# Kernel optimization log

Measured on AMD Instinct MI355X. Metric: run time of the kernel, lower is better.

The kernel has to match this reference:

```python
import jax, jax.numpy as jnp
import numpy as np
from jax import lax

B, T, V = 128, 100, 100000
ED, MD, H = 300, 50, 512   # embed_dim, mask_dim, l_hidden_size
HH = H // 2                # per-direction GRU hidden
C1 = 0.1
C2 = 0.1


def _reverse_valid(x, lens):
    # reverse the valid prefix of each sequence (emulates packed-sequence reverse dir)
    t = jnp.arange(x.shape[1])[None, :]
    idx = jnp.where(t < lens[:, None], lens[:, None] - 1 - t, t)
    return jnp.take_along_axis(x, idx[:, :, None], axis=1)


def _gru_dir(x, valid, lens, wih, whh, bih, bhh, reverse):
    # x: [B,T,Din], valid: [B,T] bool. PyTorch GRU cell math, packed-seq semantics:
    # state frozen and output zeroed at padded steps.
    if reverse:
        x = _reverse_valid(x, lens)
    h0 = jnp.zeros((x.shape[0], whh.shape[1]), x.dtype)
    def step(h, inp):
        xt, mt = inp
        gi = xt @ wih.T + bih
        gh = h @ whh.T + bhh
        ir, iz, inn = jnp.split(gi, 3, axis=-1)
        hr, hz, hn = jnp.split(gh, 3, axis=-1)
        r = jax.nn.sigmoid(ir + hr)
        z = jax.nn.sigmoid(iz + hz)
        n = jnp.tanh(inn + r * hn)
        hnew = (1.0 - z) * n + z * h
        hnew = jnp.where(mt[:, None], hnew, h)
        return hnew, jnp.where(mt[:, None], hnew, 0.0)
    _, out = lax.scan(step, h0, (x.transpose(1, 0, 2), valid.T))
    out = out.transpose(1, 0, 2)
    if reverse:
        out = _reverse_valid(out, lens)
    return out


def _crf_marginals(feats, L, trans):
    # linear-chain CRF forward-backward marginals, 2 latent states; feats [T,2], valid length L
    Tm = feats.shape[0]
    def fstep(alpha, inp):
        ft, t = inp
        new = jax.nn.logsumexp(alpha[:, None] + trans, axis=0) + ft
        a = jnp.where(t < L, new, alpha)
        return a, a
    a0 = feats[0]
    _, rest = lax.scan(fstep, a0, (feats[1:], jnp.arange(1, Tm)))
    alphas = jnp.concatenate([a0[None], rest], axis=0)
    logZ = jax.nn.logsumexp(alphas[L - 1])
    def bstep(beta, inp):
        fn, t = inp
        cand = jax.nn.logsumexp(trans + (fn + beta)[None, :], axis=1)
        b = jnp.where(t >= L - 1, jnp.zeros_like(cand), cand)
        return b, b
    _, brev = lax.scan(bstep, jnp.zeros((2,), feats.dtype), (feats[1:][::-1], jnp.arange(Tm - 2, -1, -1)))
    betas = jnp.concatenate([brev[::-1], jnp.zeros((1, 2), feats.dtype)], axis=0)
    marg = jnp.exp(alphas + betas - logZ)
    return jnp.where(jnp.arange(Tm)[:, None] < L, marg, 0.0)


def setup_inputs():
    key = jax.random.key(0)
    ks = jax.random.split(key, 30)
    s = 0.08
    inp = {}
    inp["sents"] = jax.random.randint(ks[0], (B, T), 0, V, dtype=jnp.int32)
    lens = jnp.sort(jax.random.randint(ks[1], (B,), 5, T + 1, dtype=jnp.int32))[::-1]
    inp["lens"] = lens
    t = jnp.arange(T)[None, :]
    start = (lens // 3)[:, None]
    inp["masks"] = ((t >= start) & (t < start + 3)).astype(jnp.int32)
    inp["labels"] = jax.random.randint(ks[2], (B,), 0, 3, dtype=jnp.int32)
    inp["word_emb"] = jax.random.normal(ks[3], (V, ED)) * s
    inp["mask_emb"] = jax.random.normal(ks[4], (2, MD)) * s
    i = 5
    for l, din in ((0, ED + MD), (1, H)):
        for d in ("f", "b"):
            inp[f"gru{l}{d}_wih"] = jax.random.normal(ks[i], (3 * HH, din)) * s; i += 1
            inp[f"gru{l}{d}_whh"] = jax.random.normal(ks[i], (3 * HH, HH)) * s; i += 1
            inp[f"gru{l}{d}_bih"] = jnp.zeros((3 * HH,))
            inp[f"gru{l}{d}_bhh"] = jnp.zeros((3 * HH,))
    inp["conv_w"] = jax.random.normal(ks[i], (H, H, 3)) * s; i += 1
    inp["conv_b"] = jnp.zeros((H,))
    inp["tri_w"] = jax.random.normal(ks[i], (2, 2 * H)) * s; i += 1
    inp["tri_b"] = jnp.zeros((2,))
    inp["trans"] = jax.random.normal(ks[i], (2, 2)) * s; i += 1
    inp["lab_w"] = jax.random.normal(ks[i], (3, H)) * s; i += 1
    inp["lab_b"] = jnp.zeros((3,))
    return inp


def _forward(sents, masks, labels, lens, word_emb, mask_emb, gru_params, conv_w, conv_b, tri_w, tri_b, trans, lab_w, lab_b):
    x = jnp.concatenate([word_emb[sents], mask_emb[masks]], axis=-1)  # SimpleCat
    valid = jnp.arange(T)[None, :] < lens[:, None]
    for layer in range(2):  # 2-layer bidirectional GRU
        pf, pb = gru_params[2 * layer], gru_params[2 * layer + 1]
        f = _gru_dir(x, valid, lens, *pf, False)
        b = _gru_dir(x, valid, lens, *pb, True)
        x = jnp.concatenate([f, b], axis=-1)
    context = jax.nn.relu(
        lax.conv_general_dilated(x, conv_w.transpose(2, 1, 0), (1,), [(1, 1)],
                                 dimension_numbers=("NWC", "WIO", "NWC")) + conv_b)
    mf = masks.astype(context.dtype)
    avg = jnp.einsum("bt,bth->bh", mf, context) / mf.sum(1, keepdims=True)  # target avg emb
    ctx1 = jnp.concatenate([context, jnp.broadcast_to(avg[:, None, :], context.shape)], axis=-1)
    tri = ctx1 @ tri_w.T + tri_b  # [B,T,2]
    marg = jax.vmap(_crf_marginals, in_axes=(0, 0, None))(tri, lens, trans)
    sp = marg[:, :, 1]  # select polarity, zeroed beyond each sent_len
    sent_v = jnp.einsum("bt,bth->bh", sp, context)
    gamma = jnp.clip(sp.sum(1) / 2.0, 1e-4, 1e5)
    scores = (sent_v / gamma[:, None]) @ lab_w.T + lab_b
    logp = jax.nn.log_softmax(scores, axis=-1)
    cls_loss = -jnp.mean(jnp.take_along_axis(logp, labels[:, None], axis=1))  # NLLLoss
    s_norm = jnp.mean(sp.sum(1))  # mean L1 norm of nonneg marginals
    pena = jax.nn.relu(trans[1, 0] - trans[0, 0]) + jax.nn.relu(trans[0, 1] - trans[1, 1])
    return jnp.stack([cls_loss, C1 * pena + C2 * s_norm])


def reference(sents, masks, labels, lens, word_emb, mask_emb, gru0f_wih, gru0f_whh, gru0f_bih, gru0f_bhh, gru0b_wih, gru0b_whh, gru0b_bih, gru0b_bhh, gru1f_wih, gru1f_whh, gru1f_bih, gru1f_bhh, gru1b_wih, gru1b_whh, gru1b_bih, gru1b_bhh, conv_w, conv_b, tri_w, tri_b, trans, lab_w, lab_b):
    gp = ((gru0f_wih, gru0f_whh, gru0f_bih, gru0f_bhh),
          (gru0b_wih, gru0b_whh, gru0b_bih, gru0b_bhh),
          (gru1f_wih, gru1f_whh, gru1f_bih, gru1f_bhh),
          (gru1b_wih, gru1b_whh, gru1b_bih, gru1b_bhh))
    return _forward(sents, masks, labels, lens, word_emb, mask_emb, gp, conv_w, conv_b, tri_w, tri_b, trans, lab_w, lab_b)
```

## Files before the change

kernel.cpp:

```cpp
#include <hip/hip_runtime.h>
#include <hip/hip_bf16.h>
#include <stdint.h>


#define TT 100
#define BB 128

typedef short s16;
typedef unsigned int u32;
typedef __attribute__((ext_vector_type(8))) short s16x8;
typedef __attribute__((ext_vector_type(4))) float f32x4;
typedef __attribute__((ext_vector_type(2))) float f32x2;

__device__ __forceinline__ float bf2f(s16 s) {
  return __uint_as_float(((unsigned)(unsigned short)s) << 16);
}
__device__ __forceinline__ s16 f2bf(float f) {
  __hip_bfloat16 h = __float2bfloat16(f);
  return *(s16*)&h;
}
__device__ __forceinline__ float sigf(float x) { return 1.f / (1.f + __expf(-x)); }
__device__ __forceinline__ float tanhfast(float x) { return 2.f / (1.f + __expf(-2.f * x)) - 1.f; }
__device__ __forceinline__ float lse2(float a, float b) {
  float m = fmaxf(a, b);
  return m + logf(expf(a - m) + expf(b - m));
}

__global__ void k_prep(const float* __restrict__ wih0f, const float* __restrict__ wih0b,
                       const float* __restrict__ wih1f, const float* __restrict__ wih1b,
                       const float* __restrict__ whh0f, const float* __restrict__ whh0b,
                       const float* __restrict__ whh1f, const float* __restrict__ whh1b,
                       const float* __restrict__ convw,
                       const int* __restrict__ sents, const int* __restrict__ masks,
                       const float* __restrict__ wemb, const float* __restrict__ memb,
                       s16* __restrict__ cwih0f, s16* __restrict__ cwih0b,
                       s16* __restrict__ cwih1f, s16* __restrict__ cwih1b,
                       s16* __restrict__ wf0f, s16* __restrict__ wf0b,
                       s16* __restrict__ wf1f, s16* __restrict__ wf1b,
                       s16* __restrict__ w2, s16* __restrict__ x0,
                       uint4* __restrict__ x2z) {
  const int stride = gridDim.x * 256;
  const int base = blockIdx.x * 256 + threadIdx.x;

  for (int idx = base; idx < 768 * 352; idx += stride) {
    int n = idx / 352, k = idx % 352;
    cwih0f[idx] = (k < 350) ? f2bf(wih0f[n * 350 + k]) : (s16)0;
    cwih0b[idx] = (k < 350) ? f2bf(wih0b[n * 350 + k]) : (s16)0;
  }
  for (int idx = base; idx < 393216; idx += stride) {
    cwih1f[idx] = f2bf(wih1f[idx]);
    cwih1b[idx] = f2bf(wih1b[idx]);
  }
  for (int idx = base; idx < 196608; idx += stride) {
    int w = idx / 24576, rem = idx % 24576;
    int f = rem / 512, rem2 = rem % 512;
    int l = rem2 / 8, i = rem2 % 8;
    int nt = f / 8, kt = f % 8;
    int src = (96 * w + 16 * nt + (l & 15)) * 256 + 32 * kt + 8 * (l >> 4) + i;
    wf0f[idx] = f2bf(whh0f[src]);
    wf0b[idx] = f2bf(whh0b[src]);
    wf1f[idx] = f2bf(whh1f[src]);
    wf1b[idx] = f2bf(whh1b[src]);
  }
  for (int idx = base; idx < 786432; idx += stride) {
    int o = idx / 1536, c = idx % 1536;
    int w = c / 512, i = c % 512;
    w2[idx] = f2bf(convw[o * 1536 + i * 3 + w]);
  }
  for (int idx = base; idx < BB * TT * 352; idx += stride) {
    int c = idx % 352, bt = idx / 352;
    float v;
    if (c < 300)      v = wemb[(size_t)sents[bt] * 300 + c];
    else if (c < 350) v = memb[masks[bt] * 50 + (c - 300)];
    else              v = 0.f;
    x0[idx] = f2bf(v);
  }
  for (int idx = base; idx < 819200; idx += stride)
    x2z[idx] = make_uint4(0u, 0u, 0u, 0u);
}

__global__ __launch_bounds__(256) void k_gemm(const s16* __restrict__ A, const s16* __restrict__ Bm,
                                              s16* __restrict__ C, int K, int ldA, int ldB, int ldC,
                                              const float* __restrict__ bias, int relu) {
  __shared__ s16 As[128 * 32];
  __shared__ s16 Bs[128 * 32];
  const int t = threadIdx.x, w = t >> 6, l = t & 63;
  const size_t m0 = (size_t)blockIdx.x * 128, n0 = (size_t)blockIdx.y * 128;
  f32x4 zero = {0.f, 0.f, 0.f, 0.f};
  f32x4 acc[4][4];
#pragma unroll
  for (int i = 0; i < 4; ++i)
#pragma unroll
    for (int j = 0; j < 4; ++j) acc[i][j] = zero;

  for (int kb = 0; kb < K; kb += 32) {
    __syncthreads();
    {
      const s16* gA = A + (m0 + (t >> 1)) * (size_t)ldA + kb + 16 * (t & 1);
      *(s16x8*)&As[(t >> 1) * 32 + 16 * (t & 1)]     = *(const s16x8*)gA;
      *(s16x8*)&As[(t >> 1) * 32 + 16 * (t & 1) + 8] = *(const s16x8*)(gA + 8);
      const s16* gB = Bm + (n0 + (t >> 1)) * (size_t)ldB + kb + 16 * (t & 1);
      *(s16x8*)&Bs[(t >> 1) * 32 + 16 * (t & 1)]     = *(const s16x8*)gB;
      *(s16x8*)&Bs[(t >> 1) * 32 + 16 * (t & 1) + 8] = *(const s16x8*)(gB + 8);
    }
    __syncthreads();
    s16x8 a[4], b[4];
#pragma unroll
    for (int i = 0; i < 4; ++i)
      a[i] = *(const s16x8*)&As[(64 * (w >> 1) + 16 * i + (l & 15)) * 32 + 8 * (l >> 4)];
#pragma unroll
    for (int j = 0; j < 4; ++j)
      b[j] = *(const s16x8*)&Bs[(64 * (w & 1) + 16 * j + (l & 15)) * 32 + 8 * (l >> 4)];
#pragma unroll
    for (int i = 0; i < 4; ++i)
#pragma unroll
      for (int j = 0; j < 4; ++j)
        acc[i][j] = __builtin_amdgcn_mfma_f32_16x16x32_bf16(a[i], b[j], acc[i][j], 0, 0, 0);
  }
#pragma unroll
  for (int i = 0; i < 4; ++i)
#pragma unroll
    for (int j = 0; j < 4; ++j)
#pragma unroll
      for (int r = 0; r < 4; ++r) {
        size_t row = m0 + 64 * (w >> 1) + 16 * i + 4 * (l >> 4) + r;
        size_t col = n0 + 64 * (w & 1) + 16 * j + (l & 15);
        float v = acc[i][j][r];
        if (bias) v += bias[col];
        if (relu) v = fmaxf(v, 0.f);
        C[row * (size_t)ldC + col] = f2bf(v);
      }
}

__global__ __launch_bounds__(512, 2) void k_gru(
    const s16* __restrict__ gi_f, const s16* __restrict__ gi_b,
    const s16* __restrict__ wf_f, const s16* __restrict__ wf_b,
    const float* __restrict__ bhh_f, const float* __restrict__ bhh_b,
    const int* __restrict__ lens, s16* __restrict__ out) {
  const int g = blockIdx.x;
  const int dir = blockIdx.y;
  const int tid = threadIdx.x, wid = tid >> 6, l = tid & 63;
  const s16* gi = dir ? gi_b : gi_f;
  const s16* wf = dir ? wf_b : wf_f;
  const float* bhh = dir ? bhh_b : bhh_f;
  const int col_off = dir ? 256 : 0;
  const int b0 = g * 4;

  __shared__ __align__(16) float gh2[16 * 772];
  __shared__ __align__(16) s16 hb[16 * 264];
  __shared__ int s_len[4];

  s16x8 wv[48];
#pragma unroll
  for (int f = 0; f < 48; ++f)
    wv[f] = *(const s16x8*)&wf[((size_t)(wid * 48 + f)) * 512 + l * 8];
  float bv[6];
#pragma unroll
  for (int nt = 0; nt < 6; ++nt) bv[nt] = bhh[96 * wid + 16 * nt + (l & 15)];

  for (int i = tid; i < 16 * 264; i += 512) hb[i] = 0;
  if (tid < 4) s_len[tid] = lens[b0 + tid];
  __syncthreads();

  const int smax = s_len[0];
  const int row = tid >> 7;
  const int j0 = (tid & 127) * 2;
  const int len = s_len[row];
  const s16* gbase = gi + (size_t)(b0 + row) * TT * 768 + j0;
  s16* obase = out + (size_t)(b0 + row) * TT * 512 + col_off + j0;
  float hp0 = 0.f, hp1 = 0.f;

  u32 qa0, qa1, qa2;
  int pa;
  {
    pa = dir ? (len - 1) : 0;
    const s16* gp = gbase + (size_t)pa * 768;
    qa0 = *(const u32*)gp; qa1 = *(const u32*)(gp + 256); qa2 = *(const u32*)(gp + 512);
  }

  for (int s = 0; s < smax; ++s) {
    u32 qb0 = 0, qb1 = 0, qb2 = 0;
    int pb = 0;
    if (s + 1 < len) {
      pb = dir ? (len - 2 - s) : (s + 1);
      const s16* gp = gbase + (size_t)pb * 768;
      qb0 = *(const u32*)gp; qb1 = *(const u32*)(gp + 256); qb2 = *(const u32*)(gp + 512);
    }

    f32x4 acc[6];
#pragma unroll
    for (int nt = 0; nt < 6; ++nt) { f32x4 b = {bv[nt], bv[nt], bv[nt], bv[nt]}; acc[nt] = b; }
#pragma unroll
    for (int kt = 0; kt < 8; ++kt) {
      s16x8 a = *(const s16x8*)&hb[(l & 15) * 264 + 32 * kt + 8 * (l >> 4)];
#pragma unroll
      for (int nt = 0; nt < 6; ++nt)
        acc[nt] = __builtin_amdgcn_mfma_f32_16x16x32_bf16(a, wv[nt * 8 + kt], acc[nt], 0, 0, 0);
    }
#pragma unroll
    for (int nt = 0; nt < 6; ++nt) {
      int col = 96 * wid + 16 * nt + (l & 15);
#pragma unroll
      for (int r = 0; r < 4; ++r)
        gh2[(4 * (l >> 4) + r) * 772 + col] = acc[nt][r];
    }
    __syncthreads();

    if (s < len) {
      f32x2 gr = *(const f32x2*)&gh2[row * 772 + j0];
      f32x2 gz = *(const f32x2*)&gh2[row * 772 + 256 + j0];
      f32x2 gn = *(const f32x2*)&gh2[row * 772 + 512 + j0];
      float rr0 = sigf(bf2f((s16)(qa0 & 0xffff)) + gr[0]);
      float rr1 = sigf(bf2f((s16)(qa0 >> 16))    + gr[1]);
      float zz0 = sigf(bf2f((s16)(qa1 & 0xffff)) + gz[0]);
      float zz1 = sigf(bf2f((s16)(qa1 >> 16))    + gz[1]);
      float nn0 = tanhfast(bf2f((s16)(qa2 & 0xffff)) + rr0 * gn[0]);
      float nn1 = tanhfast(bf2f((s16)(qa2 >> 16))    + rr1 * gn[1]);
      hp0 = (1.f - zz0) * nn0 + zz0 * hp0;
      hp1 = (1.f - zz1) * nn1 + zz1 * hp1;
      u32 pk = (u32)(unsigned short)f2bf(hp0) | ((u32)(unsigned short)f2bf(hp1) << 16);
      *(u32*)&hb[row * 264 + j0] = pk;
      *(u32*)&obase[(size_t)pa * 512] = pk;
    }
    __syncthreads();
    qa0 = qb0; qa1 = qb1; qa2 = qb2; pa = pb;
  }
}

__global__ void k_im2col(const s16* __restrict__ x2, s16* __restrict__ A2) {
  int idx = blockIdx.x * 256 + threadIdx.x;
  if (idx >= 2457600) return;
  size_t e = (size_t)idx * 8;
  int bt = (int)(e / 1536), c = (int)(e % 1536);
  int w = c / 512, i = c % 512;
  int b = bt / TT, t = bt % TT;
  int ts = t + w - 1;
  s16x8 v;
  if (ts >= 0 && ts < TT) v = *(const s16x8*)&x2[(size_t)(b * TT + ts) * 512 + i];
  else { s16x8 z = {0,0,0,0,0,0,0,0}; v = z; }
  *(s16x8*)&A2[e] = v;
}

__global__ void k_avg(const s16* __restrict__ ctx, const int* __restrict__ masks,
                      float* __restrict__ avg) {
  int b = blockIdx.x, t = threadIdx.x;
  float a0 = 0, a1 = 0, ms = 0;
  for (int tt = 0; tt < TT; ++tt) {
    float mf = (float)masks[b * TT + tt];
    ms += mf;
    if (mf != 0.f) {
      a0 += mf * bf2f(ctx[(size_t)(b * TT + tt) * 512 + t]);
      a1 += mf * bf2f(ctx[(size_t)(b * TT + tt) * 512 + 256 + t]);
    }
  }
  avg[b * 512 + t] = a0 / ms;
  avg[b * 512 + 256 + t] = a1 / ms;
}

__global__ void k_tri(const s16* __restrict__ ctx, const float* __restrict__ avg,
                      const float* __restrict__ triw, const float* __restrict__ trib,
                      float* __restrict__ tri) {
  int gw = (blockIdx.x * 256 + threadIdx.x) >> 6;
  int l = threadIdx.x & 63;
  if (gw >= BB * TT) return;
  int b = gw / TT;
  float a0 = 0, a1 = 0;
  for (int it = 0; it < 16; ++it) {
    int k = l + 64 * it;
    float v = (k < 512) ? bf2f(ctx[(size_t)gw * 512 + k]) : avg[b * 512 + k - 512];
    a0 += v * triw[k];
    a1 += v * triw[1024 + k];
  }
  for (int off = 32; off; off >>= 1) {
    a0 += __shfl_down(a0, off, 64);
    a1 += __shfl_down(a1, off, 64);
  }
  if (l == 0) {
    tri[gw * 2]     = a0 + trib[0];
    tri[gw * 2 + 1] = a1 + trib[1];
  }
}

__global__ void k_crf(const float* __restrict__ tri, const int* __restrict__ lens,
                      const float* __restrict__ trans, float* __restrict__ alphas,
                      float* __restrict__ sp, float* __restrict__ sp_sum) {
  int b = threadIdx.x;
  int L = lens[b];
  float t00 = trans[0], t01 = trans[1], t10 = trans[2], t11 = trans[3];
  const float* f = tri + b * 2 * TT;
  float* al = alphas + b * 2 * TT;
  float a0 = f[0], a1 = f[1];
  al[0] = a0; al[1] = a1;
  for (int t = 1; t < TT; ++t) {
    if (t < L) {
      float n0 = lse2(a0 + t00, a1 + t10) + f[2 * t];
      float n1 = lse2(a0 + t01, a1 + t11) + f[2 * t + 1];
      a0 = n0; a1 = n1;
    }
    al[2 * t] = a0; al[2 * t + 1] = a1;
  }
  float logZ = lse2(a0, a1);
  float b0 = 0.f, b1 = 0.f, ssum = 0.f;
  {
    float v = (TT - 1 < L) ? expf(al[2 * (TT - 1) + 1] - logZ) : 0.f;
    sp[b * TT + TT - 1] = v; ssum += v;
  }
  for (int t = TT - 2; t >= 0; --t) {
    float fn0 = f[2 * (t + 1)], fn1 = f[2 * (t + 1) + 1];
    float c0 = lse2(t00 + fn0 + b0, t01 + fn1 + b1);
    float c1 = lse2(t10 + fn0 + b0, t11 + fn1 + b1);
    if (t >= L - 1) { b0 = 0.f; b1 = 0.f; } else { b0 = c0; b1 = c1; }
    float v = (t < L) ? expf(al[2 * t + 1] + b1 - logZ) : 0.f;
    sp[b * TT + t] = v; ssum += v;
  }
  sp_sum[b] = ssum;
}

__global__ void k_sentv(const s16* __restrict__ ctx, const float* __restrict__ sp,
                        float* __restrict__ sv) {
  int b = blockIdx.x, t = threadIdx.x;
  float a0 = 0, a1 = 0;
  for (int tt = 0; tt < TT; ++tt) {
    float w = sp[b * TT + tt];
    if (w != 0.f) {
      a0 += w * bf2f(ctx[(size_t)(b * TT + tt) * 512 + t]);
      a1 += w * bf2f(ctx[(size_t)(b * TT + tt) * 512 + 256 + t]);
    }
  }
  sv[b * 512 + t] = a0;
  sv[b * 512 + 256 + t] = a1;
}

__global__ void k_final(const float* __restrict__ sv, const float* __restrict__ sp_sum,
                        const int* __restrict__ labels, const float* __restrict__ labw,
                        const float* __restrict__ labb, const float* __restrict__ trans,
                        float* __restrict__ out) {
  __shared__ float red[128];
  int b = threadIdx.x;
  float g = sp_sum[b] * 0.5f;
  g = fminf(fmaxf(g, 1e-4f), 1e5f);
  float s[3];
  for (int c = 0; c < 3; ++c) {
    float a = 0.f;
    for (int h = 0; h < 512; ++h) a += sv[b * 512 + h] * labw[c * 512 + h];
    s[c] = a / g + labb[c];
  }
  float m = fmaxf(s[0], fmaxf(s[1], s[2]));
  float lse = m + logf(expf(s[0] - m) + expf(s[1] - m) + expf(s[2] - m));
  red[b] = -(s[labels[b]] - lse);
  __syncthreads();
  if (b == 0) {
    float acc = 0.f, sn = 0.f;
    for (int i = 0; i < 128; ++i) { acc += red[i]; sn += sp_sum[i]; }
    float pena = fmaxf(trans[2] - trans[0], 0.f) + fmaxf(trans[1] - trans[3], 0.f);
    out[0] = acc / 128.f;
    out[1] = 0.1f * pena + 0.1f * (sn / 128.f);
  }
}

extern "C" void kernel_launch(void* const* d_in, const int* in_sizes, int n_in,
                              void* d_out, int out_size, void* d_ws, size_t ws_size,
                              hipStream_t stream) {
  const int*   sents  = (const int*)d_in[0];
  const int*   lens   = (const int*)d_in[1];
  const int*   masks  = (const int*)d_in[2];
  const int*   labels = (const int*)d_in[3];
  const float* wemb   = (const float*)d_in[4];
  const float* memb   = (const float*)d_in[5];
  const float* wih0f = (const float*)d_in[6],  *whh0f = (const float*)d_in[7];
  const float* bih0f = (const float*)d_in[8],  *bhh0f = (const float*)d_in[9];
  const float* wih0b = (const float*)d_in[10], *whh0b = (const float*)d_in[11];
  const float* bih0b = (const float*)d_in[12], *bhh0b = (const float*)d_in[13];
  const float* wih1f = (const float*)d_in[14], *whh1f = (const float*)d_in[15];
  const float* bih1f = (const float*)d_in[16], *bhh1f = (const float*)d_in[17];
  const float* wih1b = (const float*)d_in[18], *whh1b = (const float*)d_in[19];
  const float* bih1b = (const float*)d_in[20], *bhh1b = (const float*)d_in[21];
  const float* convw = (const float*)d_in[22], *convb = (const float*)d_in[23];
  const float* triw  = (const float*)d_in[24], *trib  = (const float*)d_in[25];
  const float* trans = (const float*)d_in[26];
  const float* labw  = (const float*)d_in[27], *labb  = (const float*)d_in[28];
  float* out = (float*)d_out;
  char* ws = (char*)d_ws;

  s16* x0    = (s16*)(ws + 0);
  s16* cwih0f = (s16*)(ws + 9011200);
  s16* cwih0b = (s16*)(ws + 9551872);
  s16* cwih1f = (s16*)(ws + 10092544);
  s16* cwih1b = (s16*)(ws + 10878976);
  s16* wf0f  = (s16*)(ws + 11665408);
  s16* wf0b  = (s16*)(ws + 12058624);
  s16* wf1f  = (s16*)(ws + 12451840);
  s16* wf1b  = (s16*)(ws + 12845056);
  s16* w2    = (s16*)(ws + 13238272);
  s16* giF   = (s16*)(ws + 14811136);
  s16* giB   = (s16*)(ws + 34471936);
  s16* x1    = (s16*)(ws + 54132736);
  s16* x2    = (s16*)(ws + 67239936);
  s16* A2    = giF;
  s16* ctx   = x1;
  float* avg   = (float*)(ws + 80347136);
  float* tri   = (float*)(ws + 80609280);
  float* alphas= (float*)(ws + 80711680);
  float* sp    = (float*)(ws + 80814080);
  float* spsum = (float*)(ws + 80865280);
  float* sentv = (float*)(ws + 80865792);

  k_prep<<<2048, 256, 0, stream>>>(wih0f, wih0b, wih1f, wih1b,
                                   whh0f, whh0b, whh1f, whh1b, convw,
                                   sents, masks, wemb, memb,
                                   cwih0f, cwih0b, cwih1f, cwih1b,
                                   wf0f, wf0b, wf1f, wf1b, w2, x0, (uint4*)x2);

  k_gemm<<<dim3(100, 6), 256, 0, stream>>>(x0, cwih0f, giF, 352, 352, 352, 768, bih0f, 0);
  k_gemm<<<dim3(100, 6), 256, 0, stream>>>(x0, cwih0b, giB, 352, 352, 352, 768, bih0b, 0);
  k_gru<<<dim3(32, 2), 512, 0, stream>>>(giF, giB, wf0f, wf0b, bhh0f, bhh0b, lens, x1);

  k_gemm<<<dim3(100, 6), 256, 0, stream>>>(x1, cwih1f, giF, 512, 512, 512, 768, bih1f, 0);
  k_gemm<<<dim3(100, 6), 256, 0, stream>>>(x1, cwih1b, giB, 512, 512, 512, 768, bih1b, 0);
  k_gru<<<dim3(32, 2), 512, 0, stream>>>(giF, giB, wf1f, wf1b, bhh1f, bhh1b, lens, x2);

  k_im2col<<<9600, 256, 0, stream>>>(x2, A2);
  k_gemm<<<dim3(100, 4), 256, 0, stream>>>(A2, w2, ctx, 1536, 1536, 1536, 512, convb, 1);
  k_avg<<<128, 256, 0, stream>>>(ctx, masks, avg);
  k_tri<<<3200, 256, 0, stream>>>(ctx, avg, triw, trib, tri);
  k_crf<<<1, 128, 0, stream>>>(tri, lens, trans, alphas, sp, spsum);
  k_sentv<<<128, 256, 0, stream>>>(ctx, sp, sentv);
  k_final<<<1, 128, 0, stream>>>(sentv, spsum, labels, labw, labb, trans, out);
}
```

Measured before the change: 1.010 ms.

## Interleave GRU gate columns per wave and double-buffer hidden state to drop a barrier

Recurrent weights are reordered so each wave's MFMA output columns hold the r, z and n gates of the same 32 hidden units. Each wave can then compute its own gate update right after the matmul, and the hidden state is double-buffered in shared memory, so one of the two per-step __syncthreads goes away. The r/z parts of the hidden bias are folded into the input-projection bias in the prep kernel, leaving only the n-gate bias in the recurrence. The risk is the shared gh2 staging: it is now 4 rows and is read back with no barrier or wave-level sync between the l<16 lanes' writes and the other lanes' reads, and every step waits on the lens[b0] bound.

```diff
diff --git a/kernel.cpp b/kernel.cpp
--- a/kernel.cpp
+++ b/kernel.cpp
@@ -10,7 +10,6 @@
 typedef unsigned int u32;
 typedef __attribute__((ext_vector_type(8))) short s16x8;
 typedef __attribute__((ext_vector_type(4))) float f32x4;
-typedef __attribute__((ext_vector_type(2))) float f32x2;
 
 __device__ __forceinline__ float bf2f(s16 s) {
   return __uint_as_float(((unsigned)(unsigned short)s) << 16);
@@ -33,15 +32,28 @@
                        const float* __restrict__ convw,
                        const int* __restrict__ sents, const int* __restrict__ masks,
                        const float* __restrict__ wemb, const float* __restrict__ memb,
+                       const float* __restrict__ bih0f, const float* __restrict__ bhh0f,
+                       const float* __restrict__ bih0b, const float* __restrict__ bhh0b,
+                       const float* __restrict__ bih1f, const float* __restrict__ bhh1f,
+                       const float* __restrict__ bih1b, const float* __restrict__ bhh1b,
                        s16* __restrict__ cwih0f, s16* __restrict__ cwih0b,
                        s16* __restrict__ cwih1f, s16* __restrict__ cwih1b,
                        s16* __restrict__ wf0f, s16* __restrict__ wf0b,
                        s16* __restrict__ wf1f, s16* __restrict__ wf1b,
                        s16* __restrict__ w2, s16* __restrict__ x0,
-                       uint4* __restrict__ x2z) {
+                       uint4* __restrict__ x2z,
+                       float* __restrict__ cb0f, float* __restrict__ cb0b,
+                       float* __restrict__ cb1f, float* __restrict__ cb1b) {
   const int stride = gridDim.x * 256;
   const int base = blockIdx.x * 256 + threadIdx.x;
 
+  for (int idx = base; idx < 768; idx += stride) {
+    float e = (idx < 512) ? 1.f : 0.f;
+    cb0f[idx] = bih0f[idx] + e * bhh0f[idx];
+    cb0b[idx] = bih0b[idx] + e * bhh0b[idx];
+    cb1f[idx] = bih1f[idx] + e * bhh1f[idx];
+    cb1b[idx] = bih1b[idx] + e * bhh1b[idx];
+  }
   for (int idx = base; idx < 768 * 352; idx += stride) {
     int n = idx / 352, k = idx % 352;
     cwih0f[idx] = (k < 350) ? f2bf(wih0f[n * 350 + k]) : (s16)0;
@@ -56,7 +68,9 @@
     int f = rem / 512, rem2 = rem % 512;
     int l = rem2 / 8, i = rem2 % 8;
     int nt = f / 8, kt = f % 8;
-    int src = (96 * w + 16 * nt + (l & 15)) * 256 + 32 * kt + 8 * (l >> 4) + i;
+    int jg = 16 * nt + (l & 15);
+    int jl = jg / 3, gate = jg - 3 * jl;
+    int src = (gate * 256 + 32 * w + jl) * 256 + 32 * kt + 8 * (l >> 4) + i;
     wf0f[idx] = f2bf(whh0f[src]);
     wf0b[idx] = f2bf(whh0b[src]);
     wf1f[idx] = f2bf(whh1f[src]);
@@ -146,84 +160,110 @@
   const int col_off = dir ? 256 : 0;
   const int b0 = g * 4;
 
-  __shared__ __align__(16) float gh2[16 * 772];
-  __shared__ __align__(16) s16 hb[16 * 264];
+  __shared__ __align__(16) float gh2[4 * 772];
+  __shared__ __align__(16) s16 hb[2 * 16 * 264];
   __shared__ int s_len[4];
 
   s16x8 wv[48];
 #pragma unroll
   for (int f = 0; f < 48; ++f)
     wv[f] = *(const s16x8*)&wf[((size_t)(wid * 48 + f)) * 512 + l * 8];
-  float bv[6];
-#pragma unroll
-  for (int nt = 0; nt < 6; ++nt) bv[nt] = bhh[96 * wid + 16 * nt + (l & 15)];
-
-  for (int i = tid; i < 16 * 264; i += 512) hb[i] = 0;
+
+  const int jl = l & 31;
+  const int jg = 32 * wid + jl;
+  const float bhn = bhh[512 + jg];
+
+  for (int i = tid; i < 2 * 16 * 264; i += 512) hb[i] = 0;
   if (tid < 4) s_len[tid] = lens[b0 + tid];
   __syncthreads();
 
   const int smax = s_len[0];
-  const int row = tid >> 7;
-  const int j0 = (tid & 127) * 2;
-  const int len = s_len[row];
-  const s16* gbase = gi + (size_t)(b0 + row) * TT * 768 + j0;
-  s16* obase = out + (size_t)(b0 + row) * TT * 512 + col_off + j0;
-  float hp0 = 0.f, hp1 = 0.f;
-
-  u32 qa0, qa1, qa2;
-  int pa;
-  {
-    pa = dir ? (len - 1) : 0;
-    const s16* gp = gbase + (size_t)pa * 768;
-    qa0 = *(const u32*)gp; qa1 = *(const u32*)(gp + 256); qa2 = *(const u32*)(gp + 512);
-  }
+  const int ra = l >> 5;
+  const int rb = ra + 2;
+  const int lena = s_len[ra], lenb = s_len[rb];
+  const s16* gA = gi + (size_t)(b0 + ra) * TT * 768 + jg;
+  const s16* gB = gi + (size_t)(b0 + rb) * TT * 768 + jg;
+  s16* oA = out + (size_t)(b0 + ra) * TT * 512 + col_off + jg;
+  s16* oB = out + (size_t)(b0 + rb) * TT * 512 + col_off + jg;
+  float hpa = 0.f, hpb = 0.f;
+
+  s16 qar, qaz, qan, qbr, qbz, qbn;
+  int pa = dir ? (lena - 1) : 0;
+  { const s16* gp = gA + (size_t)pa * 768; qar = gp[0]; qaz = gp[256]; qan = gp[512]; }
+  int pb = dir ? (lenb - 1) : 0;
+  { const s16* gp = gB + (size_t)pb * 768; qbr = gp[0]; qbz = gp[256]; qbn = gp[512]; }
 
   for (int s = 0; s < smax; ++s) {
-    u32 qb0 = 0, qb1 = 0, qb2 = 0;
-    int pb = 0;
-    if (s + 1 < len) {
-      pb = dir ? (len - 2 - s) : (s + 1);
-      const s16* gp = gbase + (size_t)pb * 768;
-      qb0 = *(const u32*)gp; qb1 = *(const u32*)(gp + 256); qb2 = *(const u32*)(gp + 512);
-    }
-
+    const s16* hr = hb + (s & 1) * (16 * 264);
+    s16* hw = hb + ((s + 1) & 1) * (16 * 264);
+
+    s16 nar = 0, naz = 0, nan_ = 0, nbr = 0, nbz = 0, nbn = 0;
+    int npa = 0, npb = 0;
+    if (s + 1 < lena) {
+      npa = dir ? (lena - 2 - s) : (s + 1);
+      const s16* gp = gA + (size_t)npa * 768;
+      nar = gp[0]; naz = gp[256]; nan_ = gp[512];
+    }
+    if (s + 1 < lenb) {
+      npb = dir ? (lenb - 2 - s) : (s + 1);
+      const s16* gp = gB + (size_t)npb * 768;
+      nbr = gp[0]; nbz = gp[256]; nbn = gp[512];
+    }
+
+    f32x4 zero = {0.f, 0.f, 0.f, 0.f};
     f32x4 acc[6];
 #pragma unroll
-    for (int nt = 0; nt < 6; ++nt) { f32x4 b = {bv[nt], bv[nt], bv[nt], bv[nt]}; acc[nt] = b; }
+    for (int nt = 0; nt < 6; ++nt) acc[nt] = zero;
 #pragma unroll
     for (int kt = 0; kt < 8; ++kt) {
-      s16x8 a = *(const s16x8*)&hb[(l & 15) * 264 + 32 * kt + 8 * (l >> 4)];
+      s16x8 a = *(const s16x8*)&hr[(l & 15) * 264 + 32 * kt + 8 * (l >> 4)];
 #pragma unroll
       for (int nt = 0; nt < 6; ++nt)
         acc[nt] = __builtin_amdgcn_mfma_f32_16x16x32_bf16(a, wv[nt * 8 + kt], acc[nt], 0, 0, 0);
     }
-#pragma unroll
-    for (int nt = 0; nt < 6; ++nt) {
-      int col = 96 * wid + 16 * nt + (l & 15);
-#pragma unroll
-      for (int r = 0; r < 4; ++r)
-        gh2[(4 * (l >> 4) + r) * 772 + col] = acc[nt][r];
+    if (l < 16) {
+#pragma unroll
+      for (int nt = 0; nt < 6; ++nt) {
+        int col = 96 * wid + 16 * nt + l;
+#pragma unroll
+        for (int r = 0; r < 4; ++r)
+          gh2[r * 772 + col] = acc[nt][r];
+      }
+    }
+    {
+      int cb = 96 * wid + 3 * jl;
+      if (s < lena) {
+        float g0 = gh2[ra * 772 + cb];
+        float g1 = gh2[ra * 772 + cb + 1];
+        float g2 = gh2[ra * 772 + cb + 2];
+        float rr = sigf(bf2f(qar) + g0);
+        float zz = sigf(bf2f(qaz) + g1);
+        float nn = tanhfast(bf2f(qan) + rr * (g2 + bhn));
+        hpa = (1.f - zz) * nn + zz * hpa;
+        s16 hv = f2bf(hpa);
+        hw[ra * 264 + jg] = hv;
+        oA[(size_t)pa * 512] = hv;
+      } else if (s == lena) {
+        hw[ra * 264 + jg] = f2bf(hpa);
+      }
+      if (s < lenb) {
+        float g0 = gh2[rb * 772 + cb];
+        float g1 = gh2[rb * 772 + cb + 1];
+        float g2 = gh2[rb * 772 + cb + 2];
+        float rr = sigf(bf2f(qbr) + g0);
+        float zz = sigf(bf2f(qbz) + g1);
+        float nn = tanhfast(bf2f(qbn) + rr * (g2 + bhn));
+        hpb = (1.f - zz) * nn + zz * hpb;
+        s16 hv = f2bf(hpb);
+        hw[rb * 264 + jg] = hv;
+        oB[(size_t)pb * 512] = hv;
+      } else if (s == lenb) {
+        hw[rb * 264 + jg] = f2bf(hpb);
+      }
     }
     __syncthreads();
-
-    if (s < len) {
-      f32x2 gr = *(const f32x2*)&gh2[row * 772 + j0];
-      f32x2 gz = *(const f32x2*)&gh2[row * 772 + 256 + j0];
-      f32x2 gn = *(const f32x2*)&gh2[row * 772 + 512 + j0];
-      float rr0 = sigf(bf2f((s16)(qa0 & 0xffff)) + gr[0]);
-      float rr1 = sigf(bf2f((s16)(qa0 >> 16))    + gr[1]);
-      float zz0 = sigf(bf2f((s16)(qa1 & 0xffff)) + gz[0]);
-      float zz1 = sigf(bf2f((s16)(qa1 >> 16))    + gz[1]);
-      float nn0 = tanhfast(bf2f((s16)(qa2 & 0xffff)) + rr0 * gn[0]);
-      float nn1 = tanhfast(bf2f((s16)(qa2 >> 16))    + rr1 * gn[1]);
-      hp0 = (1.f - zz0) * nn0 + zz0 * hp0;
-      hp1 = (1.f - zz1) * nn1 + zz1 * hp1;
-      u32 pk = (u32)(unsigned short)f2bf(hp0) | ((u32)(unsigned short)f2bf(hp1) << 16);
-      *(u32*)&hb[row * 264 + j0] = pk;
-      *(u32*)&obase[(size_t)pa * 512] = pk;
-    }
-    __syncthreads();
-    qa0 = qb0; qa1 = qb1; qa2 = qb2; pa = pb;
+    qar = nar; qaz = naz; qan = nan_; pa = npa;
+    qbr = nbr; qbz = nbz; qbn = nbn; pb = npb;
   }
 }
 
@@ -404,19 +444,26 @@
   float* sp    = (float*)(ws + 80814080);
   float* spsum = (float*)(ws + 80865280);
   float* sentv = (float*)(ws + 80865792);
+  float* cb0f  = (float*)(ws + 81127936);
+  float* cb0b  = (float*)(ws + 81131008);
+  float* cb1f  = (float*)(ws + 81134080);
+  float* cb1b  = (float*)(ws + 81137152);
 
   k_prep<<<2048, 256, 0, stream>>>(wih0f, wih0b, wih1f, wih1b,
                                    whh0f, whh0b, whh1f, whh1b, convw,
                                    sents, masks, wemb, memb,
+                                   bih0f, bhh0f, bih0b, bhh0b,
+                                   bih1f, bhh1f, bih1b, bhh1b,
                                    cwih0f, cwih0b, cwih1f, cwih1b,
-                                   wf0f, wf0b, wf1f, wf1b, w2, x0, (uint4*)x2);
-
-  k_gemm<<<dim3(100, 6), 256, 0, stream>>>(x0, cwih0f, giF, 352, 352, 352, 768, bih0f, 0);
-  k_gemm<<<dim3(100, 6), 256, 0, stream>>>(x0, cwih0b, giB, 352, 352, 352, 768, bih0b, 0);
+                                   wf0f, wf0b, wf1f, wf1b, w2, x0, (uint4*)x2,
+                                   cb0f, cb0b, cb1f, cb1b);
+
+  k_gemm<<<dim3(100, 6), 256, 0, stream>>>(x0, cwih0f, giF, 352, 352, 352, 768, cb0f, 0);
+  k_gemm<<<dim3(100, 6), 256, 0, stream>>>(x0, cwih0b, giB, 352, 352, 352, 768, cb0b, 0);
   k_gru<<<dim3(32, 2), 512, 0, stream>>>(giF, giB, wf0f, wf0b, bhh0f, bhh0b, lens, x1);
 
-  k_gemm<<<dim3(100, 6), 256, 0, stream>>>(x1, cwih1f, giF, 512, 512, 512, 768, bih1f, 0);
-  k_gemm<<<dim3(100, 6), 256, 0, stream>>>(x1, cwih1b, giB, 512, 512, 512, 768, bih1b, 0);
+  k_gemm<<<dim3(100, 6), 256, 0, stream>>>(x1, cwih1f, giF, 512, 512, 512, 768, cb1f, 0);
+  k_gemm<<<dim3(100, 6), 256, 0, stream>>>(x1, cwih1b, giB, 512, 512, 512, 768, cb1b, 0);
   k_gru<<<dim3(32, 2), 512, 0, stream>>>(giF, giB, wf1f, wf1b, bhh1f, bhh1b, lens, x2);
 
   k_im2col<<<9600, 256, 0, stream>>>(x2, A2);
```

Result: slower. 1.056 ms (+4.5%).
